# Performance work log

Measured on AMD Instinct MI355X. Metric: run time of the kernel, lower is better.

## Reference

```python
import jax, jax.numpy as jnp
import numpy as np

H = 128      # hidden_units
L = 200      # maxlen
B = 2048     # batch of sequences
E = 8        # num_experts
SW = 64      # switch hidden dim


def setup_inputs() -> dict:
    key = jax.random.key(0)
    ks = jax.random.split(key, 16)
    s = 0.05
    inp = {
        "x": jax.random.normal(ks[0], (B, L, H), jnp.float32),
        "x_real": jax.random.normal(ks[1], (1, L, H), jnp.float32),
        "user_embedding": jax.random.normal(ks[2], (1, H), jnp.float32),
        # uexpert: conv1d(H,H,1) -> relu -> conv1d(H,H,1); weights [out,in]
        "uW1": jax.random.normal(ks[3], (H, H), jnp.float32) * s,
        "ub1": jax.random.normal(ks[4], (H,), jnp.float32) * s,
        "uW2": jax.random.normal(ks[5], (H, H), jnp.float32) * s,
        "ub2": jax.random.normal(ks[6], (H,), jnp.float32) * s,
        # stacked expert weights [E, out, in]
        "eW1": jax.random.normal(ks[7], (E, H, H), jnp.float32) * s,
        "eb1": jax.random.normal(ks[8], (E, H), jnp.float32) * s,
        "eW2": jax.random.normal(ks[9], (E, H, H), jnp.float32) * s,
        "eb2": jax.random.normal(ks[10], (E, H), jnp.float32) * s,
        # switch MLP: H -> SW -> E
        "sW1": jax.random.normal(ks[11], (SW, H), jnp.float32) * s,
        "sb1": jax.random.normal(ks[12], (SW,), jnp.float32) * s,
        "sW2": jax.random.normal(ks[13], (E, SW), jnp.float32) * s,
        "sb2": jax.random.normal(ks[14], (E,), jnp.float32) * s,
    }
    return inp


def _ffn(x, W1, b1, W2, b2):
    # conv1d(k=1) -> (dropout: identity at eval) -> relu -> conv1d(k=1) -> dropout
    h = jax.nn.relu(jnp.einsum("blh,oh->blo", x, W1) + b1)
    return jnp.einsum("blh,oh->blo", h, W2) + b2


def reference(x, x_real, user_embedding, uW1, ub1, uW2, ub2,
              eW1, eb1, eW2, eb2, sW1, sb1, sW2, sb2):
    # client_rep == 'avg': mean over the sequence of x_real -> [H]
    x_input = jnp.mean(x_real[0], axis=0)
    # switch MLP with ReLU on all but last layer
    h = jax.nn.relu(x_input @ sW1.T + sb1)
    logits = h @ sW2.T + sb2                      # [E]
    route_prob = jax.nn.softmax(logits, axis=-1)
    route = jnp.argmax(route_prob, axis=-1)       # scalar expert index
    out_prob_max = route_prob[route]
    # selected expert branch
    expert_out = _ffn(x, eW1[route], eb1[route], eW2[route], eb2[route])
    # always-on uexpert branch
    uexpert_out = _ffn(x, uW1, ub1, uW2, ub2)
    final_output = expert_out + uexpert_out       # [B, L, H]
    return (final_output, route, out_prob_max)
```

## Files before the change

### kernel.cpp

```cpp
#include <hip/hip_runtime.h>

#define HD 128
#define LSEQ 200
#define BATCH 2048
#define NE 8
#define SWH 64

#define BM 32
#define LDX 136
#define LDH 264
#define NTILES ((BATCH * LSEQ) / BM)
#define GRID 512

typedef float f32x4 __attribute__((ext_vector_type(4)));
typedef __bf16 bf16x4 __attribute__((ext_vector_type(4)));
typedef __bf16 bf16x8 __attribute__((ext_vector_type(8)));

#define BAR() do {                                          \
    asm volatile("s_waitcnt lgkmcnt(0)" ::: "memory");      \
    __builtin_amdgcn_sched_barrier(0);                      \
    __builtin_amdgcn_s_barrier();                           \
    __builtin_amdgcn_sched_barrier(0);                      \
} while (0)

static __device__ __forceinline__ unsigned short f2bf(float f) {
    union { float f; unsigned u; } v; v.f = f;
    unsigned u = v.u;
    u += 0x7fffu + ((u >> 16) & 1u);
    return (unsigned short)(u >> 16);
}

__global__ void prep_route(const float* __restrict__ x_real,
                           const float* __restrict__ sW1, const float* __restrict__ sb1,
                           const float* __restrict__ sW2, const float* __restrict__ sb2,
                           const float* __restrict__ uW1, const float* __restrict__ ub1,
                           const float* __restrict__ uW2, const float* __restrict__ ub2,
                           const float* __restrict__ eW1, const float* __restrict__ eb1,
                           const float* __restrict__ eW2, const float* __restrict__ eb2,
                           float* __restrict__ out_tail,
                           unsigned short* __restrict__ W1c, unsigned short* __restrict__ W2c,
                           float* __restrict__ b1c, float* __restrict__ b2s) {
    __shared__ float part[256];
    __shared__ float xm[HD];
    __shared__ float hsw[SWH];
    __shared__ float logits[NE];
    __shared__ int route_s;
    const int t = threadIdx.x;

    {
        int col = t & 127, half = t >> 7;
        float s = 0.f;
        for (int l = half * 100; l < half * 100 + 100; ++l) s += x_real[l * HD + col];
        part[t] = s;
    }
    __syncthreads();
    if (t < HD) xm[t] = (part[t] + part[t + 128]) * (1.0f / LSEQ);
    __syncthreads();
    if (t < SWH) {
        float s = sb1[t];
        for (int k = 0; k < HD; ++k) s += xm[k] * sW1[t * HD + k];
        hsw[t] = s > 0.f ? s : 0.f;
    }
    __syncthreads();
    if (t < NE) {
        float s = sb2[t];
        for (int k = 0; k < SWH; ++k) s += hsw[k] * sW2[t * SWH + k];
        logits[t] = s;
    }
    __syncthreads();
    if (t == 0) {
        float mx = logits[0]; int am = 0;
        for (int e = 1; e < NE; ++e) if (logits[e] > mx) { mx = logits[e]; am = e; }
        float den = 0.f;
        for (int e = 0; e < NE; ++e) den += __expf(logits[e] - mx);
        route_s = am;
        if (blockIdx.x == 0) {
            out_tail[0] = (float)am;
            out_tail[1] = 1.0f / den;
        }
    }
    __syncthreads();
    const int r = route_s;

    const int i = blockIdx.x * 256 + t;
    if (i < 2 * HD * HD) {
        int o = i >> 7, k = i & 127;
        float v1 = (o < HD) ? uW1[o * HD + k] : eW1[r * HD * HD + (o - HD) * HD + k];
        W1c[i] = f2bf(v1);
        int o2 = i >> 8, j = i & 255;
        float v2 = (j < HD) ? uW2[o2 * HD + j] : eW2[r * HD * HD + o2 * HD + (j - HD)];
        W2c[i] = f2bf(v2);
    }
    if (i < 2 * HD) b1c[i] = (i < HD) ? ub1[i] : eb1[r * HD + (i - HD)];
    if (i < HD)     b2s[i] = ub2[i] + eb2[r * HD + i];
}

__global__ __launch_bounds__(256, 2)
void moe_main(const float* __restrict__ x,
              const unsigned short* __restrict__ W1c, const unsigned short* __restrict__ W2c,
              const float* __restrict__ b1c, const float* __restrict__ b2s,
              float* __restrict__ out) {
    __shared__ __align__(16) unsigned short xs[BM * LDX];
    __shared__ __align__(16) unsigned short hs[BM * LDH];

    const int t = threadIdx.x;
    const int lane = t & 63;
    const int w = t >> 6;
    const int l16 = lane & 15;
    const int lq = lane >> 4;
    const int ncb = w * 64;
    const int ncb2 = w * 32;

    bf16x8 w1[4][4];
    bf16x8 w2[8][2];
#pragma unroll
    for (int ks = 0; ks < 4; ++ks)
#pragma unroll
        for (int ht = 0; ht < 4; ++ht)
            w1[ks][ht] = *(const bf16x8*)&W1c[(ncb + ht * 16 + l16) * HD + ks * 32 + lq * 8];
#pragma unroll
    for (int ks = 0; ks < 8; ++ks)
#pragma unroll
        for (int ct = 0; ct < 2; ++ct)
            w2[ks][ct] = *(const bf16x8*)&W2c[(ncb2 + ct * 16 + l16) * 256 + ks * 32 + lq * 8];

    f32x4 bias1v[4], bias2v[2];
#pragma unroll
    for (int ht = 0; ht < 4; ++ht) bias1v[ht] = *(const f32x4*)&b1c[ncb + ht * 16 + lq * 4];
#pragma unroll
    for (int ct = 0; ct < 2; ++ct) bias2v[ct] = *(const f32x4*)&b2s[ncb2 + ct * 16 + lq * 4];

    int tile = blockIdx.x;
    float4 pv[4];
    {
        const float4* x4 = (const float4*)(x + (size_t)tile * (BM * HD));
#pragma unroll
        for (int i = 0; i < 4; ++i) pv[i] = x4[t + i * 256];
    }

    while (tile < NTILES) {
        const int ntile = tile + GRID;

#pragma unroll
        for (int i = 0; i < 4; ++i) {
            int idx = t + i * 256;
            int row = idx >> 5;
            int c4 = idx & 31;
            bf16x4 b;
            b[0] = (__bf16)pv[i].x; b[1] = (__bf16)pv[i].y;
            b[2] = (__bf16)pv[i].z; b[3] = (__bf16)pv[i].w;
            *(bf16x4*)&xs[row * LDX + c4 * 4] = b;
        }

        if (ntile < NTILES) {
            const float4* x4 = (const float4*)(x + (size_t)ntile * (BM * HD));
#pragma unroll
            for (int i = 0; i < 4; ++i) pv[i] = x4[t + i * 256];
        }
        BAR();

        f32x4 acc1[4][2] = {};
#pragma unroll
        for (int ks = 0; ks < 4; ++ks) {
            const int kofs = ks * 32 + lq * 8;
            bf16x8 xf[2];
#pragma unroll
            for (int tt = 0; tt < 2; ++tt)
                xf[tt] = *(const bf16x8*)&xs[(tt * 16 + l16) * LDX + kofs];
#pragma unroll
            for (int ht = 0; ht < 4; ++ht)
#pragma unroll
                for (int tt = 0; tt < 2; ++tt)
                    acc1[ht][tt] = __builtin_amdgcn_mfma_f32_16x16x32_bf16(
                        w1[ks][ht], xf[tt], acc1[ht][tt], 0, 0, 0);
        }
#pragma unroll
        for (int ht = 0; ht < 4; ++ht)
#pragma unroll
            for (int tt = 0; tt < 2; ++tt) {
                bf16x4 hv;
#pragma unroll
                for (int r = 0; r < 4; ++r) {
                    float v = acc1[ht][tt][r] + bias1v[ht][r];
                    hv[r] = (__bf16)(v > 0.f ? v : 0.f);
                }
                *(bf16x4*)&hs[(tt * 16 + l16) * LDH + ncb + ht * 16 + lq * 4] = hv;
            }
        BAR();

        f32x4 acc2[2][2] = {};
#pragma unroll
        for (int ks = 0; ks < 8; ++ks) {
            const int kofs = ks * 32 + lq * 8;
            bf16x8 hf[2];
#pragma unroll
            for (int tt = 0; tt < 2; ++tt)
                hf[tt] = *(const bf16x8*)&hs[(tt * 16 + l16) * LDH + kofs];
#pragma unroll
            for (int ct = 0; ct < 2; ++ct)
#pragma unroll
                for (int tt = 0; tt < 2; ++tt)
                    acc2[ct][tt] = __builtin_amdgcn_mfma_f32_16x16x32_bf16(
                        w2[ks][ct], hf[tt], acc2[ct][tt], 0, 0, 0);
        }
        float* outp = out + (size_t)tile * (BM * HD);
#pragma unroll
        for (int ct = 0; ct < 2; ++ct)
#pragma unroll
            for (int tt = 0; tt < 2; ++tt) {
                f32x4 o;
#pragma unroll
                for (int r = 0; r < 4; ++r) o[r] = acc2[ct][tt][r] + bias2v[ct][r];
                *(f32x4*)&outp[(size_t)(tt * 16 + l16) * HD + ncb2 + ct * 16 + lq * 4] = o;
            }

        tile = ntile;
    }
}

extern "C" void kernel_launch(void* const* d_in, const int* in_sizes, int n_in,
                              void* d_out, int out_size, void* d_ws, size_t ws_size,
                              hipStream_t stream) {
    const float* x      = (const float*)d_in[0];
    const float* x_real = (const float*)d_in[1];
    const float* uW1 = (const float*)d_in[3];
    const float* ub1 = (const float*)d_in[4];
    const float* uW2 = (const float*)d_in[5];
    const float* ub2 = (const float*)d_in[6];
    const float* eW1 = (const float*)d_in[7];
    const float* eb1 = (const float*)d_in[8];
    const float* eW2 = (const float*)d_in[9];
    const float* eb2 = (const float*)d_in[10];
    const float* sW1 = (const float*)d_in[11];
    const float* sb1 = (const float*)d_in[12];
    const float* sW2 = (const float*)d_in[13];
    const float* sb2 = (const float*)d_in[14];
    float* out = (float*)d_out;

    char* ws = (char*)d_ws;
    unsigned short* W1c = (unsigned short*)(ws + 64);
    unsigned short* W2c = (unsigned short*)(ws + 64 + 65536);
    float* b1c = (float*)(ws + 64 + 131072);
    float* b2s = (float*)(ws + 64 + 131072 + 1024);

    prep_route<<<128, 256, 0, stream>>>(x_real, sW1, sb1, sW2, sb2,
                                        uW1, ub1, uW2, ub2, eW1, eb1, eW2, eb2,
                                        out + (size_t)BATCH * LSEQ * HD,
                                        W1c, W2c, b1c, b2s);
    moe_main<<<GRID, 256, 0, stream>>>(x, W1c, W2c, b1c, b2s, out);
}
```

Before: 98.65 us.

## Software-pipeline GEMM1 and GEMM2 across tiles with double-buffered LDS

Double-buffers the x and hidden LDS tiles so that each iteration runs GEMM1 for the current tile and GEMM2 for the previous tile, with a single barrier per iteration instead of two. The goal is to cut barrier stalls and let the MFMA work of both stages interleave. In exchange LDS use roughly doubles (about 51KB per block), which may limit the two blocks per CU set by the launch bounds, and the loop runs one extra drain iteration.

```diff
diff --git a/kernel.cpp b/kernel.cpp
--- a/kernel.cpp
+++ b/kernel.cpp
@@ -100,8 +100,8 @@
               const unsigned short* __restrict__ W1c, const unsigned short* __restrict__ W2c,
               const float* __restrict__ b1c, const float* __restrict__ b2s,
               float* __restrict__ out) {
-    __shared__ __align__(16) unsigned short xs[BM * LDX];
-    __shared__ __align__(16) unsigned short hs[BM * LDH];
+    __shared__ __align__(16) unsigned short xs[2][BM * LDX];
+    __shared__ __align__(16) unsigned short hs[2][BM * LDH];
 
     const int t = threadIdx.x;
     const int lane = t & 63;
@@ -130,91 +130,111 @@
 #pragma unroll
     for (int ct = 0; ct < 2; ++ct) bias2v[ct] = *(const f32x4*)&b2s[ncb2 + ct * 16 + lq * 4];
 
-    int tile = blockIdx.x;
+    const int srow0 = t >> 5;
+    const int sc4 = (t & 31) * 4;
+
+    const int t0 = blockIdx.x;
     float4 pv[4];
     {
-        const float4* x4 = (const float4*)(x + (size_t)tile * (BM * HD));
+        const float4* x4 = (const float4*)(x + (size_t)t0 * (BM * HD));
 #pragma unroll
         for (int i = 0; i < 4; ++i) pv[i] = x4[t + i * 256];
     }
-
-    while (tile < NTILES) {
-        const int ntile = tile + GRID;
-
-#pragma unroll
-        for (int i = 0; i < 4; ++i) {
-            int idx = t + i * 256;
-            int row = idx >> 5;
-            int c4 = idx & 31;
-            bf16x4 b;
-            b[0] = (__bf16)pv[i].x; b[1] = (__bf16)pv[i].y;
-            b[2] = (__bf16)pv[i].z; b[3] = (__bf16)pv[i].w;
-            *(bf16x4*)&xs[row * LDX + c4 * 4] = b;
-        }
-
-        if (ntile < NTILES) {
-            const float4* x4 = (const float4*)(x + (size_t)ntile * (BM * HD));
-#pragma unroll
-            for (int i = 0; i < 4; ++i) pv[i] = x4[t + i * 256];
-        }
+#pragma unroll
+    for (int i = 0; i < 4; ++i) {
+        bf16x4 b;
+        b[0] = (__bf16)pv[i].x; b[1] = (__bf16)pv[i].y;
+        b[2] = (__bf16)pv[i].z; b[3] = (__bf16)pv[i].w;
+        *(bf16x4*)&xs[0][(srow0 + i * 8) * LDX + sc4] = b;
+    }
+    if (t0 + GRID < NTILES) {
+        const float4* x4 = (const float4*)(x + (size_t)(t0 + GRID) * (BM * HD));
+#pragma unroll
+        for (int i = 0; i < 4; ++i) pv[i] = x4[t + i * 256];
+    }
+    BAR();
+
+    int b = 1, q = 0;
+    for (int tile = t0; tile < NTILES + GRID; tile += GRID) {
+        if (tile < NTILES) {
+            const unsigned short* xsr = xs[b ^ 1];
+            unsigned short* hsw_ = hs[q];
+            f32x4 acc1[4][2] = {};
+#pragma unroll
+            for (int ks = 0; ks < 4; ++ks) {
+                const int kofs = ks * 32 + lq * 8;
+                bf16x8 xf[2];
+#pragma unroll
+                for (int tt = 0; tt < 2; ++tt)
+                    xf[tt] = *(const bf16x8*)&xsr[(tt * 16 + l16) * LDX + kofs];
+#pragma unroll
+                for (int ht = 0; ht < 4; ++ht)
+#pragma unroll
+                    for (int tt = 0; tt < 2; ++tt)
+                        acc1[ht][tt] = __builtin_amdgcn_mfma_f32_16x16x32_bf16(
+                            w1[ks][ht], xf[tt], acc1[ht][tt], 0, 0, 0);
+            }
+#pragma unroll
+            for (int ht = 0; ht < 4; ++ht)
+#pragma unroll
+                for (int tt = 0; tt < 2; ++tt) {
+                    bf16x4 hv;
+#pragma unroll
+                    for (int r = 0; r < 4; ++r) {
+                        float v = acc1[ht][tt][r] + bias1v[ht][r];
+                        hv[r] = (__bf16)(v > 0.f ? v : 0.f);
+                    }
+                    *(bf16x4*)&hsw_[(tt * 16 + l16) * LDH + ncb + ht * 16 + lq * 4] = hv;
+                }
+        }
+
+        if (tile > t0) {
+            const unsigned short* hsr = hs[q ^ 1];
+            f32x4 acc2[2][2] = {};
+#pragma unroll
+            for (int ks = 0; ks < 8; ++ks) {
+                const int kofs = ks * 32 + lq * 8;
+                bf16x8 hf[2];
+#pragma unroll
+                for (int tt = 0; tt < 2; ++tt)
+                    hf[tt] = *(const bf16x8*)&hsr[(tt * 16 + l16) * LDH + kofs];
+#pragma unroll
+                for (int ct = 0; ct < 2; ++ct)
+#pragma unroll
+                    for (int tt = 0; tt < 2; ++tt)
+                        acc2[ct][tt] = __builtin_amdgcn_mfma_f32_16x16x32_bf16(
+                            w2[ks][ct], hf[tt], acc2[ct][tt], 0, 0, 0);
+            }
+            float* outp = out + (size_t)(tile - GRID) * (BM * HD);
+#pragma unroll
+            for (int ct = 0; ct < 2; ++ct)
+#pragma unroll
+                for (int tt = 0; tt < 2; ++tt) {
+                    f32x4 o;
+#pragma unroll
+                    for (int r = 0; r < 4; ++r) o[r] = acc2[ct][tt][r] + bias2v[ct][r];
+                    *(f32x4*)&outp[(size_t)(tt * 16 + l16) * HD + ncb2 + ct * 16 + lq * 4] = o;
+                }
+        }
+
+        if (tile + GRID < NTILES) {
+            unsigned short* xsw = xs[b];
+#pragma unroll
+            for (int i = 0; i < 4; ++i) {
+                bf16x4 bb;
+                bb[0] = (__bf16)pv[i].x; bb[1] = (__bf16)pv[i].y;
+                bb[2] = (__bf16)pv[i].z; bb[3] = (__bf16)pv[i].w;
+                *(bf16x4*)&xsw[(srow0 + i * 8) * LDX + sc4] = bb;
+            }
+            if (tile + 2 * GRID < NTILES) {
+                const float4* x4 = (const float4*)(x + (size_t)(tile + 2 * GRID) * (BM * HD));
+#pragma unroll
+                for (int i = 0; i < 4; ++i) pv[i] = x4[t + i * 256];
+            }
+        }
+
         BAR();
-
-        f32x4 acc1[4][2] = {};
-#pragma unroll
-        for (int ks = 0; ks < 4; ++ks) {
-            const int kofs = ks * 32 + lq * 8;
-            bf16x8 xf[2];
-#pragma unroll
-            for (int tt = 0; tt < 2; ++tt)
-                xf[tt] = *(const bf16x8*)&xs[(tt * 16 + l16) * LDX + kofs];
-#pragma unroll
-            for (int ht = 0; ht < 4; ++ht)
-#pragma unroll
-                for (int tt = 0; tt < 2; ++tt)
-                    acc1[ht][tt] = __builtin_amdgcn_mfma_f32_16x16x32_bf16(
-                        w1[ks][ht], xf[tt], acc1[ht][tt], 0, 0, 0);
-        }
-#pragma unroll
-        for (int ht = 0; ht < 4; ++ht)
-#pragma unroll
-            for (int tt = 0; tt < 2; ++tt) {
-                bf16x4 hv;
-#pragma unroll
-                for (int r = 0; r < 4; ++r) {
-                    float v = acc1[ht][tt][r] + bias1v[ht][r];
-                    hv[r] = (__bf16)(v > 0.f ? v : 0.f);
-                }
-                *(bf16x4*)&hs[(tt * 16 + l16) * LDH + ncb + ht * 16 + lq * 4] = hv;
-            }
-        BAR();
-
-        f32x4 acc2[2][2] = {};
-#pragma unroll
-        for (int ks = 0; ks < 8; ++ks) {
-            const int kofs = ks * 32 + lq * 8;
-            bf16x8 hf[2];
-#pragma unroll
-            for (int tt = 0; tt < 2; ++tt)
-                hf[tt] = *(const bf16x8*)&hs[(tt * 16 + l16) * LDH + kofs];
-#pragma unroll
-            for (int ct = 0; ct < 2; ++ct)
-#pragma unroll
-                for (int tt = 0; tt < 2; ++tt)
-                    acc2[ct][tt] = __builtin_amdgcn_mfma_f32_16x16x32_bf16(
-                        w2[ks][ct], hf[tt], acc2[ct][tt], 0, 0, 0);
-        }
-        float* outp = out + (size_t)tile * (BM * HD);
-#pragma unroll
-        for (int ct = 0; ct < 2; ++ct)
-#pragma unroll
-            for (int tt = 0; tt < 2; ++tt) {
-                f32x4 o;
-#pragma unroll
-                for (int r = 0; r < 4; ++r) o[r] = acc2[ct][tt][r] + bias2v[ct][r];
-                *(f32x4*)&outp[(size_t)(tt * 16 + l16) * HD + ncb2 + ct * 16 + lq * 4] = o;
-            }
-
-        tile = ntile;
+        b ^= 1; q ^= 1;
     }
 }
 
```

New measurement: 99.89 us. Within noise of the previous version (+1.3%).

## Split each tile's output columns across 8 waves instead of 4

Applied to the files above, without the earlier changes.

Raises the block size from 256 to 512 threads, so eight waves share each 32-row tile and each wave covers half as many output columns in both GEMM stages. Per-thread register-resident weight fragments, accumulators and prefetch buffers are halved, and launch bounds now ask for more resident blocks per CU. The goal is more waves in flight to hide memory latency in this bandwidth-bound pass. In exchange, barriers now synchronise twice as many waves, and every wave still reads the full x and h tiles from LDS, so LDS read traffic per tile doubles.

```diff
diff --git a/kernel.cpp b/kernel.cpp
--- a/kernel.cpp
+++ b/kernel.cpp
@@ -95,7 +95,7 @@
     if (i < HD)     b2s[i] = ub2[i] + eb2[r * HD + i];
 }
 
-__global__ __launch_bounds__(256, 2)
+__global__ __launch_bounds__(512, 4)
 void moe_main(const float* __restrict__ x,
               const unsigned short* __restrict__ W1c, const unsigned short* __restrict__ W2c,
               const float* __restrict__ b1c, const float* __restrict__ b2s,
@@ -108,58 +108,55 @@
     const int w = t >> 6;
     const int l16 = lane & 15;
     const int lq = lane >> 4;
-    const int ncb = w * 64;
-    const int ncb2 = w * 32;
-
-    bf16x8 w1[4][4];
-    bf16x8 w2[8][2];
+    const int ncb = w * 32;
+    const int ncb2 = w * 16;
+
+    bf16x8 w1[4][2];
+    bf16x8 w2[8];
 #pragma unroll
     for (int ks = 0; ks < 4; ++ks)
 #pragma unroll
-        for (int ht = 0; ht < 4; ++ht)
+        for (int ht = 0; ht < 2; ++ht)
             w1[ks][ht] = *(const bf16x8*)&W1c[(ncb + ht * 16 + l16) * HD + ks * 32 + lq * 8];
 #pragma unroll
     for (int ks = 0; ks < 8; ++ks)
-#pragma unroll
-        for (int ct = 0; ct < 2; ++ct)
-            w2[ks][ct] = *(const bf16x8*)&W2c[(ncb2 + ct * 16 + l16) * 256 + ks * 32 + lq * 8];
-
-    f32x4 bias1v[4], bias2v[2];
-#pragma unroll
-    for (int ht = 0; ht < 4; ++ht) bias1v[ht] = *(const f32x4*)&b1c[ncb + ht * 16 + lq * 4];
-#pragma unroll
-    for (int ct = 0; ct < 2; ++ct) bias2v[ct] = *(const f32x4*)&b2s[ncb2 + ct * 16 + lq * 4];
+        w2[ks] = *(const bf16x8*)&W2c[(ncb2 + l16) * 256 + ks * 32 + lq * 8];
+
+    f32x4 bias1v[2], bias2v;
+#pragma unroll
+    for (int ht = 0; ht < 2; ++ht) bias1v[ht] = *(const f32x4*)&b1c[ncb + ht * 16 + lq * 4];
+    bias2v = *(const f32x4*)&b2s[ncb2 + lq * 4];
+
+    const int srow0 = t >> 5;
+    const int sc4 = (t & 31) * 4;
 
     int tile = blockIdx.x;
-    float4 pv[4];
+    float4 pv[2];
     {
         const float4* x4 = (const float4*)(x + (size_t)tile * (BM * HD));
 #pragma unroll
-        for (int i = 0; i < 4; ++i) pv[i] = x4[t + i * 256];
+        for (int i = 0; i < 2; ++i) pv[i] = x4[t + i * 512];
     }
 
     while (tile < NTILES) {
         const int ntile = tile + GRID;
 
 #pragma unroll
-        for (int i = 0; i < 4; ++i) {
-            int idx = t + i * 256;
-            int row = idx >> 5;
-            int c4 = idx & 31;
+        for (int i = 0; i < 2; ++i) {
             bf16x4 b;
             b[0] = (__bf16)pv[i].x; b[1] = (__bf16)pv[i].y;
             b[2] = (__bf16)pv[i].z; b[3] = (__bf16)pv[i].w;
-            *(bf16x4*)&xs[row * LDX + c4 * 4] = b;
+            *(bf16x4*)&xs[(srow0 + i * 16) * LDX + sc4] = b;
         }
 
         if (ntile < NTILES) {
             const float4* x4 = (const float4*)(x + (size_t)ntile * (BM * HD));
 #pragma unroll
-            for (int i = 0; i < 4; ++i) pv[i] = x4[t + i * 256];
+            for (int i = 0; i < 2; ++i) pv[i] = x4[t + i * 512];
         }
         BAR();
 
-        f32x4 acc1[4][2] = {};
+        f32x4 acc1[2][2] = {};
 #pragma unroll
         for (int ks = 0; ks < 4; ++ks) {
             const int kofs = ks * 32 + lq * 8;
@@ -168,14 +165,14 @@
             for (int tt = 0; tt < 2; ++tt)
                 xf[tt] = *(const bf16x8*)&xs[(tt * 16 + l16) * LDX + kofs];
 #pragma unroll
-            for (int ht = 0; ht < 4; ++ht)
+            for (int ht = 0; ht < 2; ++ht)
 #pragma unroll
                 for (int tt = 0; tt < 2; ++tt)
                     acc1[ht][tt] = __builtin_amdgcn_mfma_f32_16x16x32_bf16(
                         w1[ks][ht], xf[tt], acc1[ht][tt], 0, 0, 0);
         }
 #pragma unroll
-        for (int ht = 0; ht < 4; ++ht)
+        for (int ht = 0; ht < 2; ++ht)
 #pragma unroll
             for (int tt = 0; tt < 2; ++tt) {
                 bf16x4 hv;
@@ -188,7 +185,7 @@
             }
         BAR();
 
-        f32x4 acc2[2][2] = {};
+        f32x4 acc2[2] = {};
 #pragma unroll
         for (int ks = 0; ks < 8; ++ks) {
             const int kofs = ks * 32 + lq * 8;
@@ -197,22 +194,18 @@
             for (int tt = 0; tt < 2; ++tt)
                 hf[tt] = *(const bf16x8*)&hs[(tt * 16 + l16) * LDH + kofs];
 #pragma unroll
-            for (int ct = 0; ct < 2; ++ct)
-#pragma unroll
-                for (int tt = 0; tt < 2; ++tt)
-                    acc2[ct][tt] = __builtin_amdgcn_mfma_f32_16x16x32_bf16(
-                        w2[ks][ct], hf[tt], acc2[ct][tt], 0, 0, 0);
+            for (int tt = 0; tt < 2; ++tt)
+                acc2[tt] = __builtin_amdgcn_mfma_f32_16x16x32_bf16(
+                    w2[ks], hf[tt], acc2[tt], 0, 0, 0);
         }
         float* outp = out + (size_t)tile * (BM * HD);
 #pragma unroll
-        for (int ct = 0; ct < 2; ++ct)
-#pragma unroll
-            for (int tt = 0; tt < 2; ++tt) {
-                f32x4 o;
-#pragma unroll
-                for (int r = 0; r < 4; ++r) o[r] = acc2[ct][tt][r] + bias2v[ct][r];
-                *(f32x4*)&outp[(size_t)(tt * 16 + l16) * HD + ncb2 + ct * 16 + lq * 4] = o;
-            }
+        for (int tt = 0; tt < 2; ++tt) {
+            f32x4 o;
+#pragma unroll
+            for (int r = 0; r < 4; ++r) o[r] = acc2[tt][r] + bias2v[r];
+            *(f32x4*)&outp[(size_t)(tt * 16 + l16) * HD + ncb2 + lq * 4] = o;
+        }
 
         tile = ntile;
     }
@@ -247,5 +240,5 @@
                                         uW1, ub1, uW2, ub2, eW1, eb1, eW2, eb2,
                                         out + (size_t)BATCH * LSEQ * HD,
                                         W1c, W2c, b1c, b2s);
-    moe_main<<<GRID, 256, 0, stream>>>(x, W1c, W2c, b1c, b2s, out);
-}
+    moe_main<<<GRID, 512, 0, stream>>>(x, W1c, W2c, b1c, b2s, out);
+}
```

Result: no change. 97.24 us (-1.4%).
